# Kernel optimization log

Measured on AMD Instinct MI355X. Metric: run time of the kernel, lower is better.

Reference implementation:

```python
import jax, jax.numpy as jnp
import numpy as np

B, CIN, COUT, H, W = 4, 256, 256, 64, 64
KH, KW = 3, 3
STRIDE, PAD = 1, 1
K = KH * KW


def setup_inputs() -> dict:
    key = jax.random.key(0)
    k1, k2, k3 = jax.random.split(key, 3)
    x = jax.random.normal(k1, (B, CIN, H, W), dtype=jnp.float32)
    # small offset weights -> offsets of O(1) pixel, realistic near init
    offset_w = jax.random.normal(k2, (2 * K, CIN, KH, KW), dtype=jnp.float32) * 0.01
    offset_b = jnp.zeros((2 * K,), dtype=jnp.float32)
    dcn_w = jax.random.normal(k3, (COUT, CIN, KH, KW), dtype=jnp.float32) * (1.0 / np.sqrt(CIN * K))
    dcn_b = jnp.zeros((COUT,), dtype=jnp.float32)
    return {"x": x, "offset_w": offset_w, "offset_b": offset_b, "dcn_w": dcn_w, "dcn_b": dcn_b}


def _conv2d(x, w, b):
    y = jax.lax.conv_general_dilated(
        x, w, window_strides=(STRIDE, STRIDE),
        padding=((PAD, PAD), (PAD, PAD)),
        dimension_numbers=("NCHW", "OIHW", "NCHW"))
    return y + b[None, :, None, None]


def _bilinear_gather(x, py, px):
    """x: [B,C,H,W]; py,px: [B,K,Ho,Wo] float sample coords.
    Zero padding outside image (torchvision deform_conv2d semantics).
    Returns [B,C,K,Ho,Wo]."""
    Bb, C, Hin, Win = x.shape
    y0 = jnp.floor(py); x0 = jnp.floor(px)
    wy1 = py - y0; wx1 = px - x0
    y0i = y0.astype(jnp.int32); x0i = x0.astype(jnp.int32)
    x_flat = x.reshape(Bb, C, Hin * Win)

    def corner(yi, xi, wgt):
        valid = (yi >= 0) & (yi < Hin) & (xi >= 0) & (xi < Win)
        yc = jnp.clip(yi, 0, Hin - 1)
        xc = jnp.clip(xi, 0, Win - 1)
        idx = (yc * Win + xc).reshape(Bb, -1)  # [B, K*Ho*Wo]
        vals = jax.vmap(lambda xf, ix: jnp.take(xf, ix, axis=1))(x_flat, idx)
        vals = vals.reshape(Bb, C, *yi.shape[1:])  # [B,C,K,Ho,Wo]
        w_eff = jnp.where(valid, wgt, 0.0)[:, None]  # [B,1,K,Ho,Wo]
        return vals * w_eff

    out = corner(y0i, x0i, (1.0 - wy1) * (1.0 - wx1))
    out = out + corner(y0i, x0i + 1, (1.0 - wy1) * wx1)
    out = out + corner(y0i + 1, x0i, wy1 * (1.0 - wx1))
    out = out + corner(y0i + 1, x0i + 1, wy1 * wx1)
    return out


def _deformable_block(x, offset_w, offset_b, dcn_w, dcn_b):
    offset = _conv2d(x, offset_w, offset_b)  # [B, 2K, Ho, Wo]
    Bb, _, Ho, Wo = offset.shape
    off = offset.reshape(Bb, K, 2, Ho, Wo)
    dy, dx = off[:, :, 0], off[:, :, 1]  # torchvision: (y, x) interleaved per tap

    ky = jnp.repeat(jnp.arange(KH), KW).astype(jnp.float32)  # [K]
    kx = jnp.tile(jnp.arange(KW), KH).astype(jnp.float32)    # [K]
    base_y = (jnp.arange(Ho, dtype=jnp.float32) * STRIDE - PAD)[None, :, None] + ky[:, None, None]  # [K,Ho,1]
    base_x = (jnp.arange(Wo, dtype=jnp.float32) * STRIDE - PAD)[None, None, :] + kx[:, None, None]  # [K,1,Wo]
    py = base_y[None] + dy  # [B,K,Ho,Wo]
    px = base_x[None] + dx

    patches = _bilinear_gather(x, py, px)  # [B,C,K,Ho,Wo]
    wk = dcn_w.reshape(COUT, CIN, K)
    out = jnp.einsum("bckhw,ock->bohw", patches, wk)
    return out + dcn_b[None, :, None, None]


def reference(x, offset_w, offset_b, dcn_w, dcn_b):
    return _deformable_block(x, offset_w, offset_b, dcn_w, dcn_b)
```

## Files before the change

### kernel.cpp

```cpp
#include <hip/hip_runtime.h>

#define BB 4
#define CIN 256
#define COUT 256
#define HH 64
#define WW 64
#define KK 9
#define OC2 18
#define KTOT (CIN * KK)

typedef __attribute__((ext_vector_type(8))) _Float16 h8;
typedef __attribute__((ext_vector_type(4))) float f32x4;

static __device__ __forceinline__ h8 splat_pk(unsigned pk) {
    union { unsigned u[4]; h8 h; } s;
    s.u[0] = pk; s.u[1] = pk; s.u[2] = pk; s.u[3] = pk;
    return s.h;
}

__global__ __launch_bounds__(256) void prework_kernel(
    const float* __restrict__ x, const float* __restrict__ ow,
    const float* __restrict__ dw,
    _Float16* __restrict__ xT, _Float16* __restrict__ bp,
    _Float16* __restrict__ bow)
{
    const int bid = blockIdx.x;
    const int t = threadIdx.x;
    if (bid < 1024) {
        const int b = bid >> 8, y = (bid >> 2) & 63, c0 = (bid & 3) * 64;
        __shared__ float tile[64][65];
#pragma unroll
        for (int r = 0; r < 16; ++r) {
            int idx = r * 256 + t;
            int c = idx >> 6, w = idx & 63;
            tile[c][w] = x[(((size_t)(b * CIN + c0 + c)) << 12) + (y << 6) + w];
        }
        __syncthreads();
        const int px = t >> 2;
#pragma unroll
        for (int half = 0; half < 2; ++half) {
            int cc = (t & 3) + half * 4;
            union { _Float16 h[8]; uint4 q; } u;
#pragma unroll
            for (int j = 0; j < 8; ++j) u.h[j] = (_Float16)tile[cc * 8 + j][px];
            size_t el = (((size_t)(b << 12)) + (y << 6) + px) * 256 + c0 + cc * 8;
            *(uint4*)&xT[el] = u.q;
        }
    } else if (bid < 1312) {
        int wid = (bid - 1024) * 256 + t;
        int T = wid >> 10;
        int r = wid & 1023;
        int cotile = r >> 6, lane = r & 63;
        int co = cotile * 16 + (lane & 15);
        int kbase = T * 32 + ((lane >> 4) & 3) * 8;
        union { _Float16 h[8]; uint4 q; } u;
#pragma unroll
        for (int j = 0; j < 8; ++j) {
            int k = kbase + j;
            int c = k & 255, kk = k >> 8;
            u.h[j] = (_Float16)dw[co * KTOT + c * KK + kk];
        }
        *(uint4*)&bp[(size_t)wid * 8] = u.q;
    } else {
        int wid = (bid - 1312) * 256 + t;
        int T = wid >> 7;
        int r = wid & 127;
        int lane = r & 63;
        int oc = ((r >> 6) << 4) + (lane & 15);
        int kbase = T * 32 + ((lane >> 4) & 3) * 8;
        union { _Float16 h[8]; uint4 q; } u;
#pragma unroll
        for (int j = 0; j < 8; ++j) {
            int k = kbase + j;
            int c = k & 255, kk = k >> 8;
            u.h[j] = (oc < OC2) ? (_Float16)ow[oc * KTOT + c * KK + kk] : (_Float16)0.f;
        }
        *(uint4*)&bow[(size_t)wid * 8] = u.q;
    }
}

__global__ __launch_bounds__(512, 4) void dcn_mfma_kernel(
    const _Float16* __restrict__ xT, const _Float16* __restrict__ bow,
    const float* __restrict__ ob, const _Float16* __restrict__ bp,
    const float* __restrict__ db, float* __restrict__ out)
{
    __shared__ __align__(16) char smem[32768 + 4608 + 4608];
    _Float16 (*Asl)[4096] = (_Float16(*)[4096])smem;
    float* oscr = (float*)smem;
    uint2* twp = (uint2*)(smem + 32768);
    uint2* tih = (uint2*)(smem + 32768 + 4608);

    int P = blockIdx.x;
    int L = (P & 7) * 64 + (P >> 3);
    const int b = L >> 7;
    const int rowbase = (L & 127) * 32;

    const int tid = threadIdx.x;
    const int lane = tid & 63;
    const int wn = tid >> 6;
    const int colg = lane & 15, kg = lane >> 4;

    const char* xbyte = (const char*)(xT + ((size_t)b << 20));

    {
        f32x4 oacc[2][2];
#pragma unroll
        for (int mi = 0; mi < 2; ++mi)
#pragma unroll
            for (int nj = 0; nj < 2; ++nj) { f32x4 z = {0.f,0.f,0.f,0.f}; oacc[mi][nj] = z; }

        const int T0 = wn * 9;
#pragma unroll
        for (int i = 0; i < 9; ++i) {
            int T = T0 + i;
            int kk = T >> 3;
            int ky = kk / 3, kx = kk - 3 * (kk / 3);
            int cgo = ((T & 7) << 2) + kg;
            h8 a[2];
#pragma unroll
            for (int mi = 0; mi < 2; ++mi) {
                int pxl = rowbase + mi * 16 + colg;
                int yy = (pxl >> 6) + ky - 1, xx = (pxl & 63) + kx - 1;
                h8 v = {0,0,0,0,0,0,0,0};
                if ((unsigned)yy < HH && (unsigned)xx < WW)
                    v = *(const h8*)(xbyte + ((((yy << 6) + xx) << 9) + (cgo << 4)));
                a[mi] = v;
            }
            union { uint4 q; h8 h; } bw[2];
#pragma unroll
            for (int nj = 0; nj < 2; ++nj)
                bw[nj].q = *(const uint4*)&bow[(size_t)(((T << 1) + nj) * 64 + lane) * 8];
#pragma unroll
            for (int mi = 0; mi < 2; ++mi)
#pragma unroll
                for (int nj = 0; nj < 2; ++nj)
                    oacc[mi][nj] = __builtin_amdgcn_mfma_f32_16x16x32_f16(
                        a[mi], bw[nj].h, oacc[mi][nj], 0, 0, 0);
        }
#pragma unroll
        for (int mi = 0; mi < 2; ++mi)
#pragma unroll
            for (int nj = 0; nj < 2; ++nj) {
                int px0 = mi * 16 + kg * 4;
                int oc = nj * 16 + colg;
#pragma unroll
                for (int r = 0; r < 4; ++r)
                    oscr[(wn * 32 + px0 + r) * 32 + oc] = oacc[mi][nj][r];
            }
    }
    __syncthreads();

    if (tid < 288) {
        int e = tid;
        int p = e / 9, kk = e - (e / 9) * 9;
        float dy = ob[2 * kk], dx = ob[2 * kk + 1];
#pragma unroll
        for (int w2 = 0; w2 < 8; ++w2) {
            dy += oscr[(w2 * 32 + p) * 32 + 2 * kk];
            dx += oscr[(w2 * 32 + p) * 32 + 2 * kk + 1];
        }
        int pxl = rowbase + p;
        int y = pxl >> 6, xx = pxl & 63;
        int ky = kk / 3, kx = kk - 3 * (kk / 3);
        float sy = (float)(y - 1 + ky) + dy;
        float sx = (float)(xx - 1 + kx) + dx;
        float fy = floorf(sy), fx = floorf(sx);
        int y0 = (int)fy, x0 = (int)fx;
        float wy1 = sy - fy, wx1 = sx - fx;
        float wy0 = 1.f - wy1, wx0 = 1.f - wx1;
        bool vy0 = (unsigned)y0 < HH, vy1 = (unsigned)(y0 + 1) < HH;
        bool vx0 = (unsigned)x0 < WW, vx1 = (unsigned)(x0 + 1) < WW;
        _Float16 w00 = (_Float16)((vy0 && vx0) ? wy0 * wx0 : 0.f);
        _Float16 w01 = (_Float16)((vy0 && vx1) ? wy0 * wx1 : 0.f);
        _Float16 w10 = (_Float16)((vy1 && vx0) ? wy1 * wx0 : 0.f);
        _Float16 w11 = (_Float16)((vy1 && vx1) ? wy1 * wx1 : 0.f);
        union { _Float16 h[2]; unsigned u; } pk2;
        uint2 W;
        pk2.h[0] = w00; pk2.h[1] = w01; W.x = pk2.u;
        pk2.h[0] = w10; pk2.h[1] = w11; W.y = pk2.u;
        twp[e] = W;
        int y0c = min(max(y0, 0), HH - 1), y1c = min(max(y0 + 1, 0), HH - 1);
        int x0c = min(max(x0, 0), WW - 1), x1c = min(max(x0 + 1, 0), WW - 1);
        unsigned i00 = (unsigned)((y0c << 6) + x0c);
        unsigned i01 = (unsigned)((y0c << 6) + x1c);
        unsigned i10 = (unsigned)((y1c << 6) + x0c);
        unsigned i11 = (unsigned)((y1c << 6) + x1c);
        tih[e] = make_uint2(i00 | (i01 << 16), i10 | (i11 << 16));
    }
    __syncthreads();

    const int g_px = tid >> 4;
    const int g_cg = tid & 15;
    const int g_ebase = g_px * 9;
    const int g_w0 = g_cg * 32 + (g_px ^ (g_cg & 7));

    auto AGLOAD = [&](int st, h8* C) {
        uint2 ij = tih[g_ebase + (st >> 1)];
        unsigned chb = (unsigned)((st & 1) * 256 + g_cg * 16);
        C[0] = *(const h8*)(xbyte + (((ij.x & 0xFFFFu) << 9) + chb));
        C[1] = *(const h8*)(xbyte + (((ij.x >> 16)     << 9) + chb));
        C[2] = *(const h8*)(xbyte + (((ij.y & 0xFFFFu) << 9) + chb));
        C[3] = *(const h8*)(xbyte + (((ij.y >> 16)     << 9) + chb));
    };
    auto GCONSUME = [&](int st, int buf, const h8* C) {
        uint2 w = twp[g_ebase + (st >> 1)];
        unsigned w00 = (w.x & 0xFFFFu) * 0x10001u;
        unsigned w01 = (w.x >> 16)     * 0x10001u;
        unsigned w10 = (w.y & 0xFFFFu) * 0x10001u;
        unsigned w11 = (w.y >> 16)     * 0x10001u;
        h8 v = C[0] * splat_pk(w00);
        v += C[1] * splat_pk(w01);
        v += C[2] * splat_pk(w10);
        v += C[3] * splat_pk(w11);
        *(h8*)&Asl[buf][g_w0 * 8] = v;
    };
    auto BLOAD = [&](int st, uint4* br) {
#pragma unroll
        for (int ks = 0; ks < 4; ++ks)
#pragma unroll
            for (int nj = 0; nj < 2; ++nj) {
                size_t word = ((size_t)((st * 4 + ks) * 16 + wn * 2 + nj)) * 64 + lane;
                br[ks * 2 + nj] = *(const uint4*)&bp[word * 8];
            }
    };

    f32x4 acc[2][2];
#pragma unroll
    for (int mi = 0; mi < 2; ++mi)
#pragma unroll
        for (int nj = 0; nj < 2; ++nj) { f32x4 z = {0.f,0.f,0.f,0.f}; acc[mi][nj] = z; }

    auto MFMA16 = [&](int buf, uint4* br) {
        __builtin_amdgcn_s_setprio(1);
#pragma unroll
        for (int ks = 0; ks < 4; ++ks) {
            const int cg = ks * 4 + kg;
            union { uint4 q; h8 h; } b0, b1;
            b0.q = br[ks * 2]; b1.q = br[ks * 2 + 1];
#pragma unroll
            for (int mi = 0; mi < 2; ++mi) {
                int w = cg * 32 + ((mi * 16 + colg) ^ (cg & 7));
                h8 a = *(const h8*)&Asl[buf][w * 8];
                acc[mi][0] = __builtin_amdgcn_mfma_f32_16x16x32_f16(a, b0.h, acc[mi][0], 0, 0, 0);
                acc[mi][1] = __builtin_amdgcn_mfma_f32_16x16x32_f16(a, b1.h, acc[mi][1], 0, 0, 0);
            }
        }
        __builtin_amdgcn_s_setprio(0);
    };

    h8 C[4];
    uint4 breg[8], bnext[8];

    AGLOAD(0, C);
    BLOAD(0, breg);
    GCONSUME(0, 0, C);
    __syncthreads();

    for (int s = 0; s < 18; ++s) {
        const int cur = s & 1;
        if (s + 1 < 18) {
            AGLOAD(s + 1, C);
            BLOAD(s + 1, bnext);
        }
        MFMA16(cur, breg);
        if (s + 1 < 18) GCONSUME(s + 1, cur ^ 1, C);
        __syncthreads();
#pragma unroll
        for (int i = 0; i < 8; ++i) breg[i] = bnext[i];
    }

#pragma unroll
    for (int nj = 0; nj < 2; ++nj) {
        const int co = wn * 32 + nj * 16 + colg;
        const float bv = db[co];
        float* op = out + ((size_t)(b * COUT + co) << 12) + rowbase + kg * 4;
#pragma unroll
        for (int mi = 0; mi < 2; ++mi) {
            float4 o;
            o.x = acc[mi][nj][0] + bv;
            o.y = acc[mi][nj][1] + bv;
            o.z = acc[mi][nj][2] + bv;
            o.w = acc[mi][nj][3] + bv;
            *(float4*)&op[mi * 16] = o;
        }
    }
}

extern "C" void kernel_launch(void* const* d_in, const int* in_sizes, int n_in,
                              void* d_out, int out_size, void* d_ws, size_t ws_size,
                              hipStream_t stream)
{
    const float* x  = (const float*)d_in[0];
    const float* ow = (const float*)d_in[1];
    const float* ob = (const float*)d_in[2];
    const float* dw = (const float*)d_in[3];
    const float* db = (const float*)d_in[4];
    float* out = (float*)d_out;

    char* wsp = (char*)d_ws;
    _Float16*  bp  = (_Float16*)wsp;
    _Float16*  bow = (_Float16*)(wsp + 1179648);
    _Float16*  xT  = (_Float16*)(wsp + 1327104);

    hipLaunchKernelGGL(prework_kernel,  dim3(1348), dim3(256), 0, stream, x, ow, dw, xT, bp, bow);
    hipLaunchKernelGGL(dcn_mfma_kernel, dim3(512),  dim3(512), 0, stream, xT, bow, ob, bp, db, out);
}
```

Before: 63.43 us.

## Merge prework branches into uniform blocks and double-buffer offset-conv loads

The prework kernel is restructured so every 512-thread block transposes two x tiles and also converts a slice of the DCN and offset weights, replacing three divergent block roles with one uniform grid. In the offset conv, operand loads for the next tap are issued into a second register buffer before the current MFMAs, so load latency can overlap with compute. The offset scratch row stride is padded from 32 to 33 floats to reduce LDS bank conflicts, which grows shared memory slightly. The added registers and shared memory may lower occupancy.

```diff
diff --git a/kernel.cpp b/kernel.cpp
--- a/kernel.cpp
+++ b/kernel.cpp
@@ -18,41 +18,44 @@
     return s.h;
 }
 
-__global__ __launch_bounds__(256) void prework_kernel(
+__global__ __launch_bounds__(512) void prework_kernel(
     const float* __restrict__ x, const float* __restrict__ ow,
     const float* __restrict__ dw,
     _Float16* __restrict__ xT, _Float16* __restrict__ bp,
     _Float16* __restrict__ bow)
 {
-    const int bid = blockIdx.x;
-    const int t = threadIdx.x;
-    if (bid < 1024) {
-        const int b = bid >> 8, y = (bid >> 2) & 63, c0 = (bid & 3) * 64;
-        __shared__ float tile[64][65];
-#pragma unroll
-        for (int r = 0; r < 16; ++r) {
-            int idx = r * 256 + t;
-            int c = idx >> 6, w = idx & 63;
-            tile[c][w] = x[(((size_t)(b * CIN + c0 + c)) << 12) + (y << 6) + w];
-        }
-        __syncthreads();
-        const int px = t >> 2;
-#pragma unroll
-        for (int half = 0; half < 2; ++half) {
-            int cc = (t & 3) + half * 4;
-            union { _Float16 h[8]; uint4 q; } u;
-#pragma unroll
-            for (int j = 0; j < 8; ++j) u.h[j] = (_Float16)tile[cc * 8 + j][px];
-            size_t el = (((size_t)(b << 12)) + (y << 6) + px) * 256 + c0 + cc * 8;
-            *(uint4*)&xT[el] = u.q;
-        }
-    } else if (bid < 1312) {
-        int wid = (bid - 1024) * 256 + t;
+    __shared__ float tile[2][64][65];
+
+    const int tid = threadIdx.x;
+    const int half = tid >> 8, t = tid & 255;
+    const int chunk = (blockIdx.x << 1) + half;
+    const int tb = chunk >> 8, ty = (chunk >> 2) & 63, tc0 = (chunk & 3) * 64;
+
+#pragma unroll
+    for (int r = 0; r < 16; ++r) {
+        int idx = r * 256 + t;
+        int c = idx >> 6, w = idx & 63;
+        tile[half][c][w] = x[(((size_t)(tb * CIN + tc0 + c)) << 12) + (ty << 6) + w];
+    }
+    __syncthreads();
+    const int px = t >> 2;
+#pragma unroll
+    for (int h2 = 0; h2 < 2; ++h2) {
+        int cc = (t & 3) + h2 * 4;
+        union { _Float16 h[8]; uint4 q; } u;
+#pragma unroll
+        for (int j = 0; j < 8; ++j) u.h[j] = (_Float16)tile[half][cc * 8 + j][px];
+        size_t el = (((size_t)(tb << 12)) + (ty << 6) + px) * 256 + tc0 + cc * 8;
+        *(uint4*)&xT[el] = u.q;
+    }
+
+    if (tid < 144) {
+        int wid = blockIdx.x * 144 + tid;
         int T = wid >> 10;
         int r = wid & 1023;
-        int cotile = r >> 6, lane = r & 63;
-        int co = cotile * 16 + (lane & 15);
-        int kbase = T * 32 + ((lane >> 4) & 3) * 8;
+        int cotile = r >> 6, lane2 = r & 63;
+        int co = cotile * 16 + (lane2 & 15);
+        int kbase = T * 32 + ((lane2 >> 4) & 3) * 8;
         union { _Float16 h[8]; uint4 q; } u;
 #pragma unroll
         for (int j = 0; j < 8; ++j) {
@@ -61,13 +64,14 @@
             u.h[j] = (_Float16)dw[co * KTOT + c * KK + kk];
         }
         *(uint4*)&bp[(size_t)wid * 8] = u.q;
-    } else {
-        int wid = (bid - 1312) * 256 + t;
+    }
+    if (tid >= 256 && tid < 274) {
+        int wid = blockIdx.x * 18 + (tid - 256);
         int T = wid >> 7;
         int r = wid & 127;
-        int lane = r & 63;
-        int oc = ((r >> 6) << 4) + (lane & 15);
-        int kbase = T * 32 + ((lane >> 4) & 3) * 8;
+        int lane2 = r & 63;
+        int oc = ((r >> 6) << 4) + (lane2 & 15);
+        int kbase = T * 32 + ((lane2 >> 4) & 3) * 8;
         union { _Float16 h[8]; uint4 q; } u;
 #pragma unroll
         for (int j = 0; j < 8; ++j) {
@@ -84,11 +88,11 @@
     const float* __restrict__ ob, const _Float16* __restrict__ bp,
     const float* __restrict__ db, float* __restrict__ out)
 {
-    __shared__ __align__(16) char smem[32768 + 4608 + 4608];
+    __shared__ __align__(16) char smem[33792 + 4608 + 4608];
     _Float16 (*Asl)[4096] = (_Float16(*)[4096])smem;
     float* oscr = (float*)smem;
-    uint2* twp = (uint2*)(smem + 32768);
-    uint2* tih = (uint2*)(smem + 32768 + 4608);
+    uint2* twp = (uint2*)(smem + 33792);
+    uint2* tih = (uint2*)(smem + 33792 + 4608);
 
     int P = blockIdx.x;
     int L = (P & 7) * 64 + (P >> 3);
@@ -110,13 +114,14 @@
             for (int nj = 0; nj < 2; ++nj) { f32x4 z = {0.f,0.f,0.f,0.f}; oacc[mi][nj] = z; }
 
         const int T0 = wn * 9;
-#pragma unroll
-        for (int i = 0; i < 9; ++i) {
-            int T = T0 + i;
+
+        h8 aA[2], aB[2];
+        uint4 bwA[2], bwB[2];
+
+        auto OLOAD = [&](int T, h8* a, uint4* bw) {
             int kk = T >> 3;
             int ky = kk / 3, kx = kk - 3 * (kk / 3);
             int cgo = ((T & 7) << 2) + kg;
-            h8 a[2];
 #pragma unroll
             for (int mi = 0; mi < 2; ++mi) {
                 int pxl = rowbase + mi * 16 + colg;
@@ -126,17 +131,31 @@
                     v = *(const h8*)(xbyte + ((((yy << 6) + xx) << 9) + (cgo << 4)));
                 a[mi] = v;
             }
-            union { uint4 q; h8 h; } bw[2];
 #pragma unroll
             for (int nj = 0; nj < 2; ++nj)
-                bw[nj].q = *(const uint4*)&bow[(size_t)(((T << 1) + nj) * 64 + lane) * 8];
-#pragma unroll
-            for (int mi = 0; mi < 2; ++mi)
-#pragma unroll
-                for (int nj = 0; nj < 2; ++nj)
-                    oacc[mi][nj] = __builtin_amdgcn_mfma_f32_16x16x32_f16(
-                        a[mi], bw[nj].h, oacc[mi][nj], 0, 0, 0);
-        }
+                bw[nj] = *(const uint4*)&bow[(size_t)(((T << 1) + nj) * 64 + lane) * 8];
+        };
+        auto OMFMA = [&](const h8* a, const uint4* bw) {
+            union { uint4 q; h8 h; } b0, b1;
+            b0.q = bw[0]; b1.q = bw[1];
+#pragma unroll
+            for (int mi = 0; mi < 2; ++mi) {
+                oacc[mi][0] = __builtin_amdgcn_mfma_f32_16x16x32_f16(a[mi], b0.h, oacc[mi][0], 0, 0, 0);
+                oacc[mi][1] = __builtin_amdgcn_mfma_f32_16x16x32_f16(a[mi], b1.h, oacc[mi][1], 0, 0, 0);
+            }
+        };
+
+        OLOAD(T0, aA, bwA);
+#pragma unroll
+        for (int i = 0; i < 9; ++i) {
+            if (i + 1 < 9) {
+                if (i & 1) OLOAD(T0 + i + 1, aA, bwA);
+                else       OLOAD(T0 + i + 1, aB, bwB);
+            }
+            if (i & 1) OMFMA(aB, bwB);
+            else       OMFMA(aA, bwA);
+        }
+
 #pragma unroll
         for (int mi = 0; mi < 2; ++mi)
 #pragma unroll
@@ -145,7 +164,7 @@
                 int oc = nj * 16 + colg;
 #pragma unroll
                 for (int r = 0; r < 4; ++r)
-                    oscr[(wn * 32 + px0 + r) * 32 + oc] = oacc[mi][nj][r];
+                    oscr[(wn * 32 + px0 + r) * 33 + oc] = oacc[mi][nj][r];
             }
     }
     __syncthreads();
@@ -156,8 +175,8 @@
         float dy = ob[2 * kk], dx = ob[2 * kk + 1];
 #pragma unroll
         for (int w2 = 0; w2 < 8; ++w2) {
-            dy += oscr[(w2 * 32 + p) * 32 + 2 * kk];
-            dx += oscr[(w2 * 32 + p) * 32 + 2 * kk + 1];
+            dy += oscr[(w2 * 32 + p) * 33 + 2 * kk];
+            dx += oscr[(w2 * 32 + p) * 33 + 2 * kk + 1];
         }
         int pxl = rowbase + p;
         int y = pxl >> 6, xx = pxl & 63;
@@ -302,6 +321,6 @@
     _Float16*  bow = (_Float16*)(wsp + 1179648);
     _Float16*  xT  = (_Float16*)(wsp + 1327104);
 
-    hipLaunchKernelGGL(prework_kernel,  dim3(1348), dim3(256), 0, stream, x, ow, dw, xT, bp, bow);
-    hipLaunchKernelGGL(dcn_mfma_kernel, dim3(512),  dim3(512), 0, stream, xT, bow, ob, bp, db, out);
+    hipLaunchKernelGGL(prework_kernel,  dim3(512), dim3(512), 0, stream, x, ow, dw, xT, bp, bow);
+    hipLaunchKernelGGL(dcn_mfma_kernel, dim3(512), dim3(512), 0, stream, xT, bow, ob, bp, db, out);
 }
```

Result: faster. 62.02 us (-2.2%).
